# Kernel tuning notes

Measured on AMD Instinct MI355X. Metric: run time of the kernel, lower is better.

## Reference

```python
import jax, jax.numpy as jnp
import numpy as np

EMBED_DIM = 512
B, N = 8, 2048


def setup_inputs() -> dict:
    key = jax.random.key(0)
    ks = jax.random.split(key, 9)
    d = EMBED_DIM
    s = 1.0 / np.sqrt(d)
    return {
        "x": jax.random.normal(ks[0], (B, N, d), dtype=jnp.float32),
        "Wq": jax.random.uniform(ks[1], (d, d), jnp.float32, -s, s),
        "bq": jax.random.uniform(ks[2], (d,), jnp.float32, -s, s),
        "Wk": jax.random.uniform(ks[3], (d, d), jnp.float32, -s, s),
        "bk": jax.random.uniform(ks[4], (d,), jnp.float32, -s, s),
        "Wv": jax.random.uniform(ks[5], (d, d), jnp.float32, -s, s),
        "bv": jax.random.uniform(ks[6], (d,), jnp.float32, -s, s),
        "Wo": jax.random.uniform(ks[7], (d, d), jnp.float32, -s, s),
        "bo": jax.random.uniform(ks[8], (d,), jnp.float32, -s, s),
    }


def reference(x, Wq, bq, Wk, bk, Wv, bv, Wo, bo):
    d = x.shape[-1]
    scale = d ** (-0.5)
    q = x @ Wq + bq              # [B, N, D]
    k = x @ Wk + bk
    v = x @ Wv + bv
    attn = jnp.einsum('bnd,bmd->bnm', q, k) * scale  # [B, N, N]
    attn = jax.nn.softmax(attn, axis=-1)
    out = jnp.einsum('bnm,bmd->bnd', attn, v)
    return out @ Wo + bo
```

## Files before the change

kernel.cpp:

```cpp
#include <hip/hip_runtime.h>
#include <hip/hip_bf16.h>
#include <hip/hip_fp8.h>
#include <stdint.h>

typedef __bf16 bf16;
typedef __attribute__((ext_vector_type(8))) short short8;
typedef __attribute__((ext_vector_type(4))) float f32x4;
typedef __attribute__((ext_vector_type(4))) bf16 bf16x4;
typedef __attribute__((ext_vector_type(8))) int int8v;
typedef __attribute__((ext_vector_type(4))) int int4v;

#define DIM 512
#define NBATCH 8
#define SEQ 2048

#define VMCNT(N) asm volatile("s_waitcnt vmcnt(" #N ")" ::: "memory")
#define CFENCE   asm volatile("" ::: "memory")

__device__ __forceinline__ void gld_lds16(const void* g, void* l) {
    __builtin_amdgcn_global_load_lds(
        (const __attribute__((address_space(1))) void*)g,
        (__attribute__((address_space(3))) void*)l,
        16, 0, 0);
}

__device__ __forceinline__ unsigned char f32_to_e4m3(float v) {
#if __has_builtin(__builtin_amdgcn_cvt_pk_fp8_f32)
    return (unsigned char)(__builtin_amdgcn_cvt_pk_fp8_f32(v, v, 0, false) & 0xff);
#else
    return __hip_cvt_float_to_fp8(v, __HIP_SATFINITE, __HIP_E4M3);
#endif
}

template <int MODE, int SWIZ>
__global__ __launch_bounds__(256) void gemm_bt(
    const bf16* __restrict__ A, const bf16* __restrict__ Bt,
    void* __restrict__ Cv, uint8_t* __restrict__ Vt,
    const float* __restrict__ bias, int N, int K, int gx)
{
    __shared__ bf16 smem[32768];
    bf16* Asb = smem;
    bf16* Bsb = smem + 16384;

    int bx, by;
    {
        const unsigned g = blockIdx.x;
        const unsigned xcd = g & 7;
        const unsigned t = g >> 3;
        const unsigned per = (gridDim.x >> 3) / (unsigned)gx;
        by = xcd * per + t / (unsigned)gx;
        bx = t % (unsigned)gx;
    }

    const int tid  = threadIdx.x;
    const int lane = tid & 63;
    const int w    = tid >> 6;
    const int wr   = w >> 1;
    const int wc   = w & 1;
    const int lm   = lane & 15;
    const int lk   = lane >> 4;
    const int fs   = lm & 7;
    const int rq   = tid >> 3;
    const int pc   = tid & 7;
    const int scol = ((pc ^ (rq & 7)) * 8);

    const bf16* Ag = A + (size_t)(by * 128) * K;
    const bf16* Bg = Bt + (size_t)(bx * 128) * K;

    f32x4 acc[4][4];
#pragma unroll
    for (int i = 0; i < 4; ++i)
#pragma unroll
        for (int j = 0; j < 4; ++j)
            acc[i][j] = (f32x4){0.f, 0.f, 0.f, 0.f};

    auto stage = [&](int kb, int buf) {
#pragma unroll
        for (int t = 0; t < 4; ++t) {
            const int r = t * 32 + rq;
            gld_lds16(Ag + (size_t)r * K + kb + scol,
                      Asb + buf * 8192 + t * 2048 + tid * 8);
            gld_lds16(Bg + (size_t)r * K + kb + scol,
                      Bsb + buf * 8192 + t * 2048 + tid * 8);
        }
    };
    auto compute = [&](int buf) {
        const bf16* Ab = Asb + buf * 8192;
        const bf16* Bb = Bsb + buf * 8192;
#pragma unroll
        for (int s = 0; s < 2; ++s) {
            const int u = ((s * 4 + lk) ^ fs) * 8;
            short8 fa[4], fb[4];
#pragma unroll
            for (int i = 0; i < 4; ++i)
                fa[i] = *(const short8*)&Ab[(wr * 64 + i * 16 + lm) * 64 + u];
#pragma unroll
            for (int j = 0; j < 4; ++j)
                fb[j] = *(const short8*)&Bb[(wc * 64 + j * 16 + lm) * 64 + u];
#pragma unroll
            for (int i = 0; i < 4; ++i)
#pragma unroll
                for (int j = 0; j < 4; ++j)
                    acc[i][j] = __builtin_amdgcn_mfma_f32_16x16x32_bf16(
                        fa[i], fb[j], acc[i][j], 0, 0, 0);
        }
    };

    stage(0, 0);
    const int E = K >> 6;
#pragma unroll 2
    for (int e = 0; e < E; ++e) {
        const int p = e & 1;
        CFENCE;
        __builtin_amdgcn_s_barrier();
        CFENCE;
        if (e + 1 < E) { stage((e + 1) << 6, p ^ 1); VMCNT(8); }
        else           { VMCNT(0); }
        CFENCE;
        __builtin_amdgcn_s_barrier();
        CFENCE;
        __builtin_amdgcn_s_setprio(1);
        compute(p);
        __builtin_amdgcn_s_setprio(0);
    }
    __syncthreads();

#pragma unroll
    for (int i = 0; i < 4; ++i)
#pragma unroll
        for (int j = 0; j < 4; ++j) {
            const int col = bx * 128 + wc * 64 + j * 16 + lm;
            const float bv = bias[col];
#pragma unroll
            for (int r = 0; r < 4; ++r)
                acc[i][j][r] += bv;
        }

    if (MODE == 2) {
        float* ft = (float*)smem;
        float* outp = (float*)Cv;
#pragma unroll
        for (int h = 0; h < 2; ++h) {
            if (wr == h) {
#pragma unroll
                for (int i = 0; i < 4; ++i)
#pragma unroll
                    for (int j = 0; j < 4; ++j)
#pragma unroll
                        for (int r = 0; r < 4; ++r)
                            ft[(i * 16 + lk * 4 + r) * 132 + wc * 64 + j * 16 + lm] =
                                acc[i][j][r];
            }
            __syncthreads();
            const int rr = tid >> 5, cc = (tid & 31) * 4;
#pragma unroll
            for (int p = 0; p < 8; ++p) {
                const int row = p * 8 + rr;
                *(float4*)&outp[(size_t)(by * 128 + h * 64 + row) * N +
                                bx * 128 + cc] = *(const float4*)&ft[row * 132 + cc];
            }
            __syncthreads();
        }
        return;
    }

    const int sub  = (bx * 128) >> 9;
    const int col0 = (bx * 128) & 511;

    if (sub == 2) {
        const int b  = (by * 128) >> 11;
        const int n0 = (by * 128) & 2047;
        uint8_t* t8 = (uint8_t*)smem;
#pragma unroll
        for (int i = 0; i < 4; ++i)
#pragma unroll
            for (int j = 0; j < 4; ++j)
#pragma unroll
                for (int r = 0; r < 4; ++r) {
                    const int fl = wc * 64 + j * 16 + lm;
                    const int nl = wr * 64 + i * 16 + lk * 4 + r;
                    t8[fl * 144 + nl] = f32_to_e4m3(32.0f * acc[i][j][r]);
                }
        __syncthreads();
        const int f = tid >> 1, nh = (tid & 1) * 64;
#pragma unroll
        for (int p = 0; p < 4; ++p) {
            const uint4 raw = *(const uint4*)&t8[f * 144 + nh + p * 16];
            *(uint4*)&Vt[((size_t)(b * 512 + col0 + f)) * 2048 +
                         n0 + nh + p * 16] = raw;
        }
        return;
    }

    uint8_t* d8 = (uint8_t*)Cv + (size_t)sub * 8388608;
    uint8_t* t8 = (uint8_t*)smem;
#pragma unroll
    for (int h = 0; h < 2; ++h) {
        if (wr == h) {
#pragma unroll
            for (int i = 0; i < 4; ++i)
#pragma unroll
                for (int j = 0; j < 4; ++j)
#pragma unroll
                    for (int r = 0; r < 4; ++r)
                        t8[(i * 16 + lk * 4 + r) * 144 + wc * 64 + j * 16 + lm] =
                            f32_to_e4m3(32.0f * acc[i][j][r]);
        }
        __syncthreads();
        const int rr = tid >> 3, cc = (tid & 7) * 16;
#pragma unroll
        for (int p = 0; p < 2; ++p) {
            const int row = p * 32 + rr;
            const uint4 raw = *(const uint4*)&t8[row * 144 + cc];
            *(uint4*)&d8[(size_t)(by * 128 + h * 64 + row) * 512 + col0 + cc] =
                raw;
        }
        __syncthreads();
    }
}

template <int MODE, int E>
__global__ __launch_bounds__(256) void gemm_mx(
    const uint8_t* __restrict__ A, const uint8_t* __restrict__ Bt,
    void* __restrict__ Cv, float* __restrict__ rsum,
    int N, int K, long long sA, long long sB, long long sC, float alpha,
    int gx)
{
    __shared__ uint8_t smem[65536];
    uint8_t* Asb = smem;
    uint8_t* Bsb = smem + 32768;

    int bx, by, bz;
    {
        const unsigned g = blockIdx.x;
        bz = g & 7;
        const unsigned r = g >> 3;
        bx = r % (unsigned)gx;
        by = r / (unsigned)gx;
    }

    const int tid  = threadIdx.x;
    const int lane = tid & 63;
    const int w    = tid >> 6;
    const int wr   = w >> 1;
    const int wc   = w & 1;
    const int lm   = lane & 15;
    const int lk   = lane >> 4;
    const int rq   = tid >> 3;
    const int pc   = tid & 7;
    const int ssrc = (pc ^ (rq & 7)) * 16;
    const int ca   = ((2 * lk) ^ (lm & 7)) * 16;
    const int cb   = ((2 * lk + 1) ^ (lm & 7)) * 16;

    const size_t z = bz;
    const uint8_t* Ag = A + z * (size_t)sA + (size_t)(by * 128) * K;
    const uint8_t* Bg = Bt + z * (size_t)sB + (size_t)(bx * 128) * K;

    f32x4 acc[4][4];
#pragma unroll
    for (int i = 0; i < 4; ++i)
#pragma unroll
        for (int j = 0; j < 4; ++j)
            acc[i][j] = (f32x4){0.f, 0.f, 0.f, 0.f};

    auto stageA = [&](int kb, int buf) {
#pragma unroll
        for (int t = 0; t < 4; ++t) {
            const int r = t * 32 + rq;
            gld_lds16(Ag + (size_t)r * K + kb + ssrc,
                      Asb + buf * 16384 + t * 4096 + tid * 16);
        }
    };
    auto stageB02 = [&](int kb, int buf) {
#pragma unroll
        for (int t = 0; t < 4; t += 2) {
            const int r = t * 32 + rq;
            gld_lds16(Bg + (size_t)r * K + kb + ssrc,
                      Bsb + buf * 16384 + t * 4096 + tid * 16);
        }
    };
    auto stageB13 = [&](int kb, int buf) {
#pragma unroll
        for (int t = 1; t < 4; t += 2) {
            const int r = t * 32 + rq;
            gld_lds16(Bg + (size_t)r * K + kb + ssrc,
                      Bsb + buf * 16384 + t * 4096 + tid * 16);
        }
    };
    auto loadB = [&](const uint8_t* Bs, int j) -> int8v {
        const uint8_t* rp = Bs + (wc * 64 + j * 16 + lm) * 128;
        const int4v lo = *(const int4v*)(rp + ca);
        const int4v hi = *(const int4v*)(rp + cb);
        return (int8v){lo[0], lo[1], lo[2], lo[3], hi[0], hi[1], hi[2], hi[3]};
    };

    stageA(0, 0); stageB02(0, 0); stageB13(0, 0);

#pragma unroll
    for (int e = 0; e < E; ++e) {
        const int p = e & 1;
        const uint8_t* As = Asb + p * 16384;
        const uint8_t* Bs = Bsb + p * 16384;

        VMCNT(2);
        __builtin_amdgcn_s_barrier();
        if (e + 1 < E) {
            stageA((e + 1) * 128, p ^ 1);
            stageB02((e + 1) * 128, p ^ 1);
            stageB13((e + 1) * 128, p ^ 1);
        }
        int8v fa[4];
#pragma unroll
        for (int i = 0; i < 4; ++i) {
            const uint8_t* rp = As + (wr * 64 + i * 16 + lm) * 128;
            const int4v lo = *(const int4v*)(rp + ca);
            const int4v hi = *(const int4v*)(rp + cb);
            fa[i] = (int8v){lo[0], lo[1], lo[2], lo[3],
                            hi[0], hi[1], hi[2], hi[3]};
        }
        __builtin_amdgcn_s_setprio(1);
#pragma unroll
        for (int j = 0; j < 2; ++j) {
            const int8v fb = loadB(Bs, j);
#pragma unroll
            for (int i = 0; i < 4; ++i)
                acc[i][j] = __builtin_amdgcn_mfma_scale_f32_16x16x128_f8f6f4(
                    fa[i], fb, acc[i][j], 0, 0, 0, 127, 0, 127);
        }
        __builtin_amdgcn_s_setprio(0);

        if (e + 1 < E) { VMCNT(8); } else { VMCNT(0); }
        __builtin_amdgcn_s_barrier();
        __builtin_amdgcn_s_setprio(1);
#pragma unroll
        for (int j = 2; j < 4; ++j) {
            const int8v fb = loadB(Bs, j);
#pragma unroll
            for (int i = 0; i < 4; ++i)
                acc[i][j] = __builtin_amdgcn_mfma_scale_f32_16x16x128_f8f6f4(
                    fa[i], fb, acc[i][j], 0, 0, 0, 127, 0, 127);
        }
        __builtin_amdgcn_s_setprio(0);
    }
    __syncthreads();

    const int orow0 = by * 128 + wr * 64;

    if (MODE == 4) {
#pragma unroll
        for (int i = 0; i < 4; ++i) {
            float psum[4] = {0.f, 0.f, 0.f, 0.f};
#pragma unroll
            for (int j = 0; j < 4; ++j)
#pragma unroll
                for (int r = 0; r < 4; ++r) {
                    const float e = __expf(acc[i][j][r] * alpha);
                    acc[i][j][r] = e;
                    psum[r] += e;
                }
#pragma unroll
            for (int m = 1; m < 16; m <<= 1)
#pragma unroll
                for (int r = 0; r < 4; ++r) psum[r] += __shfl_xor(psum[r], m);
            if (lm == 0) {
#pragma unroll
                for (int r = 0; r < 4; ++r)
                    atomicAdd(&rsum[z * SEQ + orow0 + i * 16 + lk * 4 + r],
                              psum[r]);
            }
        }
        uint8_t* dst = (uint8_t*)Cv + z * (size_t)sC;
#pragma unroll
        for (int h = 0; h < 2; ++h) {
            if (wr == h) {
#pragma unroll
                for (int i = 0; i < 4; ++i)
#pragma unroll
                    for (int j = 0; j < 4; ++j)
#pragma unroll
                        for (int r = 0; r < 4; ++r)
                            smem[(i * 16 + lk * 4 + r) * 144 +
                                 wc * 64 + j * 16 + lm] =
                                f32_to_e4m3(acc[i][j][r]);
            }
            __syncthreads();
            const int rr = tid >> 3, cc = (tid & 7) * 16;
#pragma unroll
            for (int p = 0; p < 2; ++p) {
                const int row = p * 32 + rr;
                const uint4 raw = *(const uint4*)&smem[row * 144 + cc];
                *(uint4*)&dst[(size_t)(by * 128 + h * 64 + row) * N +
                              bx * 128 + cc] = raw;
            }
            __syncthreads();
        }
        return;
    }

#pragma unroll
    for (int i = 0; i < 4; ++i) {
        float inv[4];
#pragma unroll
        for (int r = 0; r < 4; ++r)
            inv[r] = 1.0f / (32.0f * rsum[z * SEQ + orow0 + i * 16 + lk * 4 + r]);
#pragma unroll
        for (int j = 0; j < 4; ++j)
#pragma unroll
            for (int r = 0; r < 4; ++r)
                acc[i][j][r] *= inv[r];
    }
    bf16* dst = (bf16*)Cv + z * (size_t)sC;
    bf16* tile = (bf16*)smem;
#pragma unroll
    for (int h = 0; h < 2; ++h) {
        if (wr == h) {
#pragma unroll
            for (int i = 0; i < 4; ++i)
#pragma unroll
                for (int j = 0; j < 4; ++j)
#pragma unroll
                    for (int r = 0; r < 4; ++r)
                        tile[(i * 16 + lk * 4 + r) * 136 + wc * 64 + j * 16 + lm] =
                            (bf16)acc[i][j][r];
        }
        __syncthreads();
        const int rr0 = tid >> 4, cc = (tid & 15) * 8;
#pragma unroll
        for (int p = 0; p < 4; ++p) {
            const int row = p * 16 + rr0;
            const uint4 raw = *(const uint4*)&tile[row * 136 + cc];
            *(uint4*)&dst[(size_t)(by * 128 + h * 64 + row) * N + bx * 128 + cc] =
                raw;
        }
        __syncthreads();
    }
}

__global__ __launch_bounds__(256) void cvt_f32_bf16(
    const float* __restrict__ x, bf16* __restrict__ o, int n4)
{
    const int i = blockIdx.x * 256 + threadIdx.x;
    if (i >= n4) return;
    const float4 v = ((const float4*)x)[i];
    bf16x4 b;
    b[0] = (bf16)v.x; b[1] = (bf16)v.y; b[2] = (bf16)v.z; b[3] = (bf16)v.w;
    ((bf16x4*)o)[i] = b;
}

__global__ __launch_bounds__(256) void transpose4(
    const float* __restrict__ Wq, const float* __restrict__ Wk,
    const float* __restrict__ Wv, const float* __restrict__ Wo,
    bf16* __restrict__ Wcat, bf16* __restrict__ Wto,
    const float* __restrict__ bq, const float* __restrict__ bk,
    const float* __restrict__ bv, float* __restrict__ bcat,
    float* __restrict__ rowsum)
{
    const int widx = blockIdx.z;
    const int t0 = threadIdx.x;
    if (widx == 4) {
        const int idx = (blockIdx.y * 8 + blockIdx.x) * 256 + t0;
        rowsum[idx] = 0.0f;
        if (idx < 1536)
            bcat[idx] = (idx < 512) ? bq[idx]
                      : (idx < 1024) ? bk[idx - 512] : bv[idx - 1024];
        return;
    }
    __shared__ bf16 tile[64][65];
    const float* W = (widx == 0) ? Wq : (widx == 1) ? Wk : (widx == 2) ? Wv : Wo;
    bf16* dst = (widx < 3) ? (Wcat + (size_t)widx * 512 * 512) : Wto;
    const int tx = blockIdx.x, ty = blockIdx.y;
#pragma unroll
    for (int it = 0; it < 16; ++it) {
        const int e = it * 256 + t0;
        const int r = e >> 6, c = e & 63;
        tile[r][c] = (bf16)W[(size_t)(ty * 64 + r) * 512 + tx * 64 + c];
    }
    __syncthreads();
#pragma unroll
    for (int it = 0; it < 16; ++it) {
        const int e = it * 256 + t0;
        const int o = e >> 6, i = e & 63;
        dst[(size_t)(tx * 64 + o) * 512 + ty * 64 + i] = tile[i][o];
    }
}

extern "C" void kernel_launch(void* const* d_in, const int* in_sizes, int n_in,
                              void* d_out, int out_size, void* d_ws, size_t ws_size,
                              hipStream_t stream)
{
    const float* x  = (const float*)d_in[0];
    const float* Wq = (const float*)d_in[1];
    const float* bq = (const float*)d_in[2];
    const float* Wk = (const float*)d_in[3];
    const float* bk = (const float*)d_in[4];
    const float* Wv = (const float*)d_in[5];
    const float* bv = (const float*)d_in[6];
    const float* Wo = (const float*)d_in[7];
    const float* bo = (const float*)d_in[8];
    float* out = (float*)d_out;

    char* ws = (char*)d_ws;
    bf16*    Xb     = (bf16*)(ws);
    bf16*    Ctx    = (bf16*)(ws);
    bf16*    Wcat   = (bf16*)(ws + 16777216);
    bf16*    Wto    = (bf16*)(ws + 18350080);
    float*   bcat   = (float*)(ws + 18874368);
    float*   rowsum = (float*)(ws + 18880512);
    uint8_t* Q8     = (uint8_t*)(ws + 20971520);
    uint8_t* K8     = (uint8_t*)(ws + 29360128);
    uint8_t* Vt8    = (uint8_t*)(ws + 54525952);
    uint8_t* S8     = (uint8_t*)(ws + 62914560);

    transpose4<<<dim3(8, 8, 5), 256, 0, stream>>>(
        Wq, Wk, Wv, Wo, Wcat, Wto, bq, bk, bv, bcat, rowsum);
    cvt_f32_bf16<<<8192, 256, 0, stream>>>(x, Xb, 2097152);

    const float scale = 0.044194173824159216f;

    gemm_bt<3, 2><<<1536, 256, 0, stream>>>(
        Xb, Wcat, Q8, Vt8, bcat, 1536, 512, 12);

    gemm_mx<4, 4><<<2048, 256, 0, stream>>>(
        Q8, K8, S8, rowsum, 2048, 512,
        2048LL * 512, 2048LL * 512, 2048LL * 2048, scale / 1024.0f, 16);

    gemm_mx<5, 16><<<512, 256, 0, stream>>>(
        S8, Vt8, Ctx, rowsum, 512, 2048,
        2048LL * 2048, 512LL * 2048, 2048LL * 512, 1.0f, 4);

    gemm_bt<2, 2><<<512, 256, 0, stream>>>(
        Ctx, Wto, out, nullptr, bo, 512, 512, 4);
}
```

Before: 213.3 us.

## Single-buffer A tile in non-softmax GEMM modes to cut LDS to 48KB

For GEMM modes other than the softmax mode, the A operand is now single-buffered in shared memory while B stays double-buffered, dropping LDS use from 64KB to 48KB per block. A fragments are read into registers before an extra barrier, after which the next A and B tiles are prefetched. The aim is more resident blocks per CU and so better latency hiding. The cost is a second barrier per k-step and a full vmcnt(0) wait, which reduces load/compute overlap.

```diff
diff --git a/kernel.cpp b/kernel.cpp
--- a/kernel.cpp
+++ b/kernel.cpp
@@ -15,6 +15,7 @@
 #define SEQ 2048
 
 #define VMCNT(N) asm volatile("s_waitcnt vmcnt(" #N ")" ::: "memory")
+#define LGKMCNT0 asm volatile("s_waitcnt lgkmcnt(0)" ::: "memory")
 #define CFENCE   asm volatile("" ::: "memory")
 
 __device__ __forceinline__ void gld_lds16(const void* g, void* l) {
@@ -226,9 +227,8 @@
     int N, int K, long long sA, long long sB, long long sC, float alpha,
     int gx)
 {
-    __shared__ uint8_t smem[65536];
-    uint8_t* Asb = smem;
-    uint8_t* Bsb = smem + 32768;
+    constexpr int SMEM_BYTES = (MODE == 4) ? 65536 : 49152;
+    __shared__ uint8_t smem[SMEM_BYTES];
 
     int bx, by, bz;
     {
@@ -263,84 +263,145 @@
         for (int j = 0; j < 4; ++j)
             acc[i][j] = (f32x4){0.f, 0.f, 0.f, 0.f};
 
-    auto stageA = [&](int kb, int buf) {
-#pragma unroll
-        for (int t = 0; t < 4; ++t) {
-            const int r = t * 32 + rq;
-            gld_lds16(Ag + (size_t)r * K + kb + ssrc,
-                      Asb + buf * 16384 + t * 4096 + tid * 16);
-        }
-    };
-    auto stageB02 = [&](int kb, int buf) {
-#pragma unroll
-        for (int t = 0; t < 4; t += 2) {
-            const int r = t * 32 + rq;
-            gld_lds16(Bg + (size_t)r * K + kb + ssrc,
-                      Bsb + buf * 16384 + t * 4096 + tid * 16);
-        }
-    };
-    auto stageB13 = [&](int kb, int buf) {
-#pragma unroll
-        for (int t = 1; t < 4; t += 2) {
-            const int r = t * 32 + rq;
-            gld_lds16(Bg + (size_t)r * K + kb + ssrc,
-                      Bsb + buf * 16384 + t * 4096 + tid * 16);
-        }
-    };
-    auto loadB = [&](const uint8_t* Bs, int j) -> int8v {
-        const uint8_t* rp = Bs + (wc * 64 + j * 16 + lm) * 128;
-        const int4v lo = *(const int4v*)(rp + ca);
-        const int4v hi = *(const int4v*)(rp + cb);
-        return (int8v){lo[0], lo[1], lo[2], lo[3], hi[0], hi[1], hi[2], hi[3]};
-    };
-
-    stageA(0, 0); stageB02(0, 0); stageB13(0, 0);
-
-#pragma unroll
-    for (int e = 0; e < E; ++e) {
-        const int p = e & 1;
-        const uint8_t* As = Asb + p * 16384;
-        const uint8_t* Bs = Bsb + p * 16384;
-
-        VMCNT(2);
-        __builtin_amdgcn_s_barrier();
-        if (e + 1 < E) {
-            stageA((e + 1) * 128, p ^ 1);
-            stageB02((e + 1) * 128, p ^ 1);
-            stageB13((e + 1) * 128, p ^ 1);
-        }
-        int8v fa[4];
-#pragma unroll
-        for (int i = 0; i < 4; ++i) {
-            const uint8_t* rp = As + (wr * 64 + i * 16 + lm) * 128;
+    if constexpr (MODE == 4) {
+        uint8_t* Asb = smem;
+        uint8_t* Bsb = smem + 32768;
+        auto stageA = [&](int kb, int buf) {
+#pragma unroll
+            for (int t = 0; t < 4; ++t) {
+                const int r = t * 32 + rq;
+                gld_lds16(Ag + (size_t)r * K + kb + ssrc,
+                          Asb + buf * 16384 + t * 4096 + tid * 16);
+            }
+        };
+        auto stageB02 = [&](int kb, int buf) {
+#pragma unroll
+            for (int t = 0; t < 4; t += 2) {
+                const int r = t * 32 + rq;
+                gld_lds16(Bg + (size_t)r * K + kb + ssrc,
+                          Bsb + buf * 16384 + t * 4096 + tid * 16);
+            }
+        };
+        auto stageB13 = [&](int kb, int buf) {
+#pragma unroll
+            for (int t = 1; t < 4; t += 2) {
+                const int r = t * 32 + rq;
+                gld_lds16(Bg + (size_t)r * K + kb + ssrc,
+                          Bsb + buf * 16384 + t * 4096 + tid * 16);
+            }
+        };
+        auto loadB = [&](const uint8_t* Bs, int j) -> int8v {
+            const uint8_t* rp = Bs + (wc * 64 + j * 16 + lm) * 128;
             const int4v lo = *(const int4v*)(rp + ca);
             const int4v hi = *(const int4v*)(rp + cb);
-            fa[i] = (int8v){lo[0], lo[1], lo[2], lo[3],
-                            hi[0], hi[1], hi[2], hi[3]};
-        }
-        __builtin_amdgcn_s_setprio(1);
-#pragma unroll
-        for (int j = 0; j < 2; ++j) {
-            const int8v fb = loadB(Bs, j);
-#pragma unroll
-            for (int i = 0; i < 4; ++i)
-                acc[i][j] = __builtin_amdgcn_mfma_scale_f32_16x16x128_f8f6f4(
-                    fa[i], fb, acc[i][j], 0, 0, 0, 127, 0, 127);
-        }
-        __builtin_amdgcn_s_setprio(0);
-
-        if (e + 1 < E) { VMCNT(8); } else { VMCNT(0); }
-        __builtin_amdgcn_s_barrier();
-        __builtin_amdgcn_s_setprio(1);
-#pragma unroll
-        for (int j = 2; j < 4; ++j) {
-            const int8v fb = loadB(Bs, j);
-#pragma unroll
-            for (int i = 0; i < 4; ++i)
-                acc[i][j] = __builtin_amdgcn_mfma_scale_f32_16x16x128_f8f6f4(
-                    fa[i], fb, acc[i][j], 0, 0, 0, 127, 0, 127);
-        }
-        __builtin_amdgcn_s_setprio(0);
+            return (int8v){lo[0], lo[1], lo[2], lo[3],
+                           hi[0], hi[1], hi[2], hi[3]};
+        };
+
+        stageA(0, 0); stageB02(0, 0); stageB13(0, 0);
+#pragma unroll
+        for (int e = 0; e < E; ++e) {
+            const int p = e & 1;
+            const uint8_t* As = Asb + p * 16384;
+            const uint8_t* Bs = Bsb + p * 16384;
+
+            VMCNT(2);
+            __builtin_amdgcn_s_barrier();
+            if (e + 1 < E) {
+                stageA((e + 1) * 128, p ^ 1);
+                stageB02((e + 1) * 128, p ^ 1);
+                stageB13((e + 1) * 128, p ^ 1);
+            }
+            int8v fa[4];
+#pragma unroll
+            for (int i = 0; i < 4; ++i) {
+                const uint8_t* rp = As + (wr * 64 + i * 16 + lm) * 128;
+                const int4v lo = *(const int4v*)(rp + ca);
+                const int4v hi = *(const int4v*)(rp + cb);
+                fa[i] = (int8v){lo[0], lo[1], lo[2], lo[3],
+                                hi[0], hi[1], hi[2], hi[3]};
+            }
+            __builtin_amdgcn_s_setprio(1);
+#pragma unroll
+            for (int j = 0; j < 2; ++j) {
+                const int8v fb = loadB(Bs, j);
+#pragma unroll
+                for (int i = 0; i < 4; ++i)
+                    acc[i][j] = __builtin_amdgcn_mfma_scale_f32_16x16x128_f8f6f4(
+                        fa[i], fb, acc[i][j], 0, 0, 0, 127, 0, 127);
+            }
+            __builtin_amdgcn_s_setprio(0);
+
+            if (e + 1 < E) { VMCNT(8); } else { VMCNT(0); }
+            __builtin_amdgcn_s_barrier();
+            __builtin_amdgcn_s_setprio(1);
+#pragma unroll
+            for (int j = 2; j < 4; ++j) {
+                const int8v fb = loadB(Bs, j);
+#pragma unroll
+                for (int i = 0; i < 4; ++i)
+                    acc[i][j] = __builtin_amdgcn_mfma_scale_f32_16x16x128_f8f6f4(
+                        fa[i], fb, acc[i][j], 0, 0, 0, 127, 0, 127);
+            }
+            __builtin_amdgcn_s_setprio(0);
+        }
+    } else {
+        uint8_t* Ab  = smem;
+        uint8_t* Bsb = smem + 16384;
+        auto stageA = [&](int kb) {
+#pragma unroll
+            for (int t = 0; t < 4; ++t) {
+                const int r = t * 32 + rq;
+                gld_lds16(Ag + (size_t)r * K + kb + ssrc,
+                          Ab + t * 4096 + tid * 16);
+            }
+        };
+        auto stageB = [&](int kb, int buf) {
+#pragma unroll
+            for (int t = 0; t < 4; ++t) {
+                const int r = t * 32 + rq;
+                gld_lds16(Bg + (size_t)r * K + kb + ssrc,
+                          Bsb + buf * 16384 + t * 4096 + tid * 16);
+            }
+        };
+
+        stageA(0); stageB(0, 0);
+#pragma unroll
+        for (int e = 0; e < E; ++e) {
+            const int p = e & 1;
+            VMCNT(0);
+            __builtin_amdgcn_s_barrier();
+            CFENCE;
+            int8v fa[4];
+#pragma unroll
+            for (int i = 0; i < 4; ++i) {
+                const uint8_t* rp = Ab + (wr * 64 + i * 16 + lm) * 128;
+                const int4v lo = *(const int4v*)(rp + ca);
+                const int4v hi = *(const int4v*)(rp + cb);
+                fa[i] = (int8v){lo[0], lo[1], lo[2], lo[3],
+                                hi[0], hi[1], hi[2], hi[3]};
+            }
+            LGKMCNT0;
+            __builtin_amdgcn_sched_barrier(0);
+            __builtin_amdgcn_s_barrier();
+            CFENCE;
+            if (e + 1 < E) { stageA((e + 1) * 128); stageB((e + 1) * 128, p ^ 1); }
+            const uint8_t* Bs = Bsb + p * 16384;
+            __builtin_amdgcn_s_setprio(1);
+#pragma unroll
+            for (int j = 0; j < 4; ++j) {
+                const uint8_t* rp = Bs + (wc * 64 + j * 16 + lm) * 128;
+                const int4v lo = *(const int4v*)(rp + ca);
+                const int4v hi = *(const int4v*)(rp + cb);
+                const int8v fb = (int8v){lo[0], lo[1], lo[2], lo[3],
+                                         hi[0], hi[1], hi[2], hi[3]};
+#pragma unroll
+                for (int i = 0; i < 4; ++i)
+                    acc[i][j] = __builtin_amdgcn_mfma_scale_f32_16x16x128_f8f6f4(
+                        fa[i], fb, acc[i][j], 0, 0, 0, 127, 0, 127);
+            }
+            __builtin_amdgcn_s_setprio(0);
+        }
     }
     __syncthreads();
 
```

After: 216.0 us. About the same (+1.3%).
